# Kernel optimization log

Measured on AMD Instinct MI355X. Metric: run time of the kernel, lower is better.

Reference implementation:

```python
import jax, jax.numpy as jnp
import numpy as np

B, N, D = 8, 8192, 3
C = 64
M = 2048          # num_samples
K = 32            # max_neighbors
RADIUS = 0.3
OUT = 128
EXP = 4
CIN = C + D       # 67
HID = CIN * EXP   # 268
EPS = 1e-6        # flax LayerNorm default


def setup_inputs() -> dict:
    key = jax.random.key(0)
    ks = jax.random.split(key, 6)
    return {
        "x": jax.random.normal(ks[0], (B, N, D), jnp.float32),
        "features": jax.random.normal(ks[1], (B, N, C), jnp.float32),
        "first_idx": jax.random.randint(ks[2], (B,), 0, N, jnp.int32),
        "w1": jax.random.normal(ks[3], (CIN, HID), jnp.float32) / np.float32(np.sqrt(CIN)),
        "b1": jnp.zeros((HID,), jnp.float32),
        "g1": jnp.ones((HID,), jnp.float32),
        "be1": jnp.zeros((HID,), jnp.float32),
        "w2": jax.random.normal(ks[4], (HID, OUT), jnp.float32) / np.float32(np.sqrt(HID)),
        "b2": jnp.zeros((OUT,), jnp.float32),
        "g2": jnp.ones((OUT,), jnp.float32),
        "be2": jnp.zeros((OUT,), jnp.float32),
    }


def _layernorm(h, g, b):
    mu = jnp.mean(h, axis=-1, keepdims=True)
    var = jnp.mean(jnp.square(h), axis=-1, keepdims=True) - jnp.square(mu)
    return (h - mu) * jax.lax.rsqrt(var + EPS) * g + b


def _fps(x, first_idx, num_samples):
    # Sequential farthest-point sampling via lax.scan.
    batch = jnp.arange(x.shape[0])
    sel = jnp.full((x.shape[0], num_samples), -1, dtype=jnp.int32)
    sel = sel.at[:, 0].set(first_idx)
    first_pts = x[batch, first_idx]                       # (B,3)
    dists = jnp.sum((x - first_pts[:, None, :]) ** 2, -1)  # (B,N)

    def step(carry, i):
        s, d = carry
        far = jnp.argmax(d, axis=-1)
        s = s.at[:, i].set(far.astype(jnp.int32))
        fp = x[batch, far]
        d = jnp.minimum(d, jnp.sum((x - fp[:, None, :]) ** 2, -1))
        return (s, d), None

    (sel, _), _ = jax.lax.scan(step, (sel, dists), jnp.arange(1, num_samples))
    return sel


def _ball_query(centers, points, radius, max_neighbors):
    # centers (B,M,3), points (B,N,3) -> (B,M,K) indices, -1 where invalid
    d2 = jnp.sum((centers[:, :, None, :] - points[:, None, :, :]) ** 2, -1)  # (B,M,N)
    within = d2 < radius ** 2
    nbr = jnp.argsort(jnp.where(within, d2, 1e10), axis=-1)[:, :, :max_neighbors]
    nd = jnp.take_along_axis(d2, nbr, axis=-1)
    return jnp.where(nd < radius ** 2, nbr, -1)


def reference(x, features, first_idx, w1, b1, g1, be1, w2, b2, g2, be2):
    batch = jnp.arange(B)[:, None]                 # (B,1)
    sel = _fps(x, first_idx, M)                    # (B,M)
    centers = x[batch, sel]                        # (B,M,3)
    nbr = _ball_query(centers, x, RADIUS, K)       # (B,M,K); -1 wraps to last point (as original)
    bI = batch[:, :, None]                         # (B,1,1)
    nf = features[bI, nbr]                         # (B,M,K,C)
    npts = x[bI, nbr]                              # (B,M,K,3)
    rel = npts - centers[:, :, None, :]
    comb = jnp.concatenate([nf, rel], axis=-1)     # (B,M,K,C+3)
    h = jax.nn.gelu(comb @ w1 + b1)                # (B,M,K,HID), tanh-approx gelu as flax default
    h = _layernorm(h, g1, be1)
    h = h @ w2 + b2                                # (B,M,K,OUT)
    h = _layernorm(h, g2, be2)
    out = jnp.max(h, axis=2)                       # (B,M,OUT)
    return (centers, out)
```

## Files before the change

kernel.cpp:

```cpp
#include <hip/hip_runtime.h>
#include <hip/hip_bf16.h>
#include <math.h>

#define B_ 8
#define N_ 8192
#define C_ 64
#define M_ 2048
#define K_ 32
#define OUT_ 128
#define CIN_ 67
#define HID_ 268
#define EPS_ 1e-6f
#define CONS_ 240
#define CAPQ_ 512

typedef short short8 __attribute__((ext_vector_type(8)));
typedef float floatx4 __attribute__((ext_vector_type(4)));

__device__ __forceinline__ unsigned short f2bf(float f) {
  unsigned u = __builtin_bit_cast(unsigned, f);
  u += 0x7fffu + ((u >> 16) & 1u);
  return (unsigned short)(u >> 16);
}
__device__ __forceinline__ float bf2f(unsigned short h) {
  return __builtin_bit_cast(float, (unsigned)h << 16);
}

__device__ __forceinline__ float d2fma(float ax, float ay, float az,
                                       float bx, float by, float bz) {
#pragma clang fp contract(off)
  float dx = ax - bx, dy = ay - by, dz = az - bz;
  return __builtin_fmaf(dz, dz, __builtin_fmaf(dy, dy, dx * dx));
}

__device__ __forceinline__ float gelu_tanh(float v) {
  const float k0 = 0.7978845608028654f;
  const float k1 = 0.044715f;
  float u = k0 * (v + k1 * v * v * v);
  return 0.5f * v * (1.0f + tanhf(u));
}

__device__ __forceinline__ int msp4(int v) {
  return (v & 1) | ((v & 2) << 2) | ((v & 4) << 4) | ((v & 8) << 6);
}

template <int CTRL>
__device__ __forceinline__ unsigned long long dpp_umax64(unsigned long long k) {
  int lo = (int)(unsigned)k;
  int hi = (int)(unsigned)(k >> 32);
  unsigned slo = (unsigned)__builtin_amdgcn_update_dpp(0, lo, CTRL, 0xF, 0xF, true);
  unsigned shi = (unsigned)__builtin_amdgcn_update_dpp(0, hi, CTRL, 0xF, 0xF, true);
  unsigned long long o = ((unsigned long long)shi << 32) | (unsigned long long)slo;
  return k > o ? k : o;
}

__global__ __launch_bounds__(256) void pack_kernel(
    const float* __restrict__ w1, const float* __restrict__ w2,
    unsigned short* __restrict__ w1p, unsigned short* __restrict__ w2p,
    int* __restrict__ prog) {
  if (blockIdx.x == 0) prog[threadIdx.x] = 0;
  int e = blockIdx.x * 256 + threadIdx.x;
  if (e < 3 * 17 * 64 * 8) {
    int j = e & 7, lane = (e >> 3) & 63, fi = e >> 9;
    int kt = fi / 17, nt = fi - kt * 17;
    int k = kt * 32 + (lane >> 4) * 8 + j;
    int n = nt * 16 + (lane & 15);
    float v = (k < CIN_ && n < HID_) ? w1[k * HID_ + n] : 0.f;
    w1p[e] = f2bf(v);
  } else {
    int e2 = e - 3 * 17 * 64 * 8;
    if (e2 < 9 * 8 * 64 * 8) {
      int j = e2 & 7, lane = (e2 >> 3) & 63, fi = e2 >> 9;
      int kt = fi >> 3, nt = fi & 7;
      int k = kt * 32 + (lane >> 4) * 8 + j;
      int n = nt * 16 + (lane & 15);
      float v = (k < HID_) ? w2[k * OUT_ + n] : 0.f;
      w2p[e2] = f2bf(v);
    }
  }
}

__global__ __launch_bounds__(512) void fused_kernel(
    const float* __restrict__ x, const float* __restrict__ features,
    const int* __restrict__ first_idx,
    const unsigned short* __restrict__ w1p, const float* __restrict__ b1,
    const float* __restrict__ g1, const float* __restrict__ be1,
    const unsigned short* __restrict__ w2p, const float* __restrict__ b2,
    const float* __restrict__ g2, const float* __restrict__ be2,
    float* __restrict__ centers, float* __restrict__ out1,
    int* __restrict__ prog) {
  __shared__ __align__(16) char smem[131456];
  const int tid = threadIdx.x;
  const int lane = tid & 63;
  const int wv = tid >> 6;

  if (blockIdx.x < B_) {
    const int b = blockIdx.x;
    const float* xb = x + (size_t)b * N_ * 3;

    float* s_xyz = (float*)smem;
    char* s_mem = smem + 98304;
    unsigned long long* s_wkey = (unsigned long long*)(smem + 131072);
    int* s_wsum = (int*)(smem + 131200);
    float* s_bb = (float*)(smem + 131232);

    int* s_hist = (int*)s_mem;
    unsigned short* s_perm = (unsigned short*)(s_mem + 16384);
    float* s_cbuf = (float*)s_mem;

    {
      const float4* src = (const float4*)xb;
      float4* dst = (float4*)s_xyz;
#pragma unroll
      for (int i = 0; i < 12; ++i) {
        int e = tid + i * 512;
        dst[e] = src[e];
      }
    }
    for (int i = tid; i < 4096; i += 512) s_hist[i] = 0;
    __syncthreads();

    float bx0 = INFINITY, bx1 = -INFINITY, by0 = INFINITY, by1 = -INFINITY,
          bz0 = INFINITY, bz1 = -INFINITY;
#pragma unroll
    for (int i = 0; i < 16; ++i) {
      int p = tid + i * 512;
      float X = s_xyz[p * 3 + 0], Y = s_xyz[p * 3 + 1], Z = s_xyz[p * 3 + 2];
      bx0 = fminf(bx0, X); bx1 = fmaxf(bx1, X);
      by0 = fminf(by0, Y); by1 = fmaxf(by1, Y);
      bz0 = fminf(bz0, Z); bz1 = fmaxf(bz1, Z);
    }
#pragma unroll
    for (int off = 1; off < 64; off <<= 1) {
      bx0 = fminf(bx0, __shfl_xor(bx0, off)); bx1 = fmaxf(bx1, __shfl_xor(bx1, off));
      by0 = fminf(by0, __shfl_xor(by0, off)); by1 = fmaxf(by1, __shfl_xor(by1, off));
      bz0 = fminf(bz0, __shfl_xor(bz0, off)); bz1 = fmaxf(bz1, __shfl_xor(bz1, off));
    }
    if (lane == 0) {
      s_bb[wv * 6 + 0] = bx0; s_bb[wv * 6 + 1] = bx1; s_bb[wv * 6 + 2] = by0;
      s_bb[wv * 6 + 3] = by1; s_bb[wv * 6 + 4] = bz0; s_bb[wv * 6 + 5] = bz1;
    }
    __syncthreads();
#pragma unroll
    for (int w = 0; w < 8; ++w) {
      bx0 = fminf(bx0, s_bb[w * 6 + 0]); bx1 = fmaxf(bx1, s_bb[w * 6 + 1]);
      by0 = fminf(by0, s_bb[w * 6 + 2]); by1 = fmaxf(by1, s_bb[w * 6 + 3]);
      bz0 = fminf(bz0, s_bb[w * 6 + 4]); bz1 = fmaxf(bz1, s_bb[w * 6 + 5]);
    }
    const float kS = 16.0f * (1.0f - 1e-6f);
    float rx = bx1 - bx0, ry = by1 - by0, rz = bz1 - bz0;
    float sxv = rx > 0.f ? kS / rx : 0.f;
    float syv = ry > 0.f ? kS / ry : 0.f;
    float szv = rz > 0.f ? kS / rz : 0.f;

#pragma unroll
    for (int i = 0; i < 16; ++i) {
      int p = tid + i * 512;
      int qx = (int)((s_xyz[p * 3 + 0] - bx0) * sxv);
      int qy = (int)((s_xyz[p * 3 + 1] - by0) * syv);
      int qz = (int)((s_xyz[p * 3 + 2] - bz0) * szv);
      qx = qx < 0 ? 0 : (qx > 15 ? 15 : qx);
      qy = qy < 0 ? 0 : (qy > 15 ? 15 : qy);
      qz = qz < 0 ? 0 : (qz > 15 ? 15 : qz);
      int c = msp4(qx) | (msp4(qy) << 1) | (msp4(qz) << 2);
      atomicAdd(&s_hist[c], 1);
    }
    __syncthreads();

    {
      int h[8], pre[8];
      int acc = 0;
#pragma unroll
      for (int i = 0; i < 8; ++i) { h[i] = s_hist[tid * 8 + i]; pre[i] = acc; acc += h[i]; }
      int incl = acc;
#pragma unroll
      for (int off = 1; off < 64; off <<= 1) {
        int v = __shfl_up(incl, off);
        if (lane >= off) incl += v;
      }
      int texcl = incl - acc;
      if (lane == 63) s_wsum[wv] = incl;
      __syncthreads();
      int woff = 0;
#pragma unroll
      for (int w = 0; w < 8; ++w) woff += (w < wv) ? s_wsum[w] : 0;
#pragma unroll
      for (int i = 0; i < 8; ++i) s_hist[tid * 8 + i] = woff + texcl + pre[i];
    }
    __syncthreads();

#pragma unroll
    for (int i = 0; i < 16; ++i) {
      int p = tid + i * 512;
      int qx = (int)((s_xyz[p * 3 + 0] - bx0) * sxv);
      int qy = (int)((s_xyz[p * 3 + 1] - by0) * syv);
      int qz = (int)((s_xyz[p * 3 + 2] - bz0) * szv);
      qx = qx < 0 ? 0 : (qx > 15 ? 15 : qx);
      qy = qy < 0 ? 0 : (qy > 15 ? 15 : qy);
      qz = qz < 0 ? 0 : (qz > 15 ? 15 : qz);
      int c = msp4(qx) | (msp4(qy) << 1) | (msp4(qz) << 2);
      int pos = atomicAdd(&s_hist[c], 1);
      s_perm[pos] = (unsigned short)p;
    }
    __syncthreads();

    float px[16], py[16], pz[16], d[16];
    unsigned lo32[16];
    float gx0[2], gx1[2], gy0[2], gy1[2], gz0[2], gz1[2];
#pragma unroll
    for (int g = 0; g < 2; ++g) {
      gx0[g] = INFINITY; gx1[g] = -INFINITY; gy0[g] = INFINITY;
      gy1[g] = -INFINITY; gz0[g] = INFINITY; gz1[g] = -INFINITY;
    }
#pragma unroll
    for (int i = 0; i < 16; ++i) {
      int p = (int)s_perm[tid * 16 + i];
      int g = i >> 3;
      px[i] = s_xyz[p * 3 + 0];
      py[i] = s_xyz[p * 3 + 1];
      pz[i] = s_xyz[p * 3 + 2];
      d[i] = INFINITY;
      lo32[i] = 0xFFFFFFFFu - (unsigned)p;
      gx0[g] = fminf(gx0[g], px[i]); gx1[g] = fmaxf(gx1[g], px[i]);
      gy0[g] = fminf(gy0[g], py[i]); gy1[g] = fmaxf(gy1[g], py[i]);
      gz0[g] = fminf(gz0[g], pz[i]); gz1[g] = fmaxf(gz1[g], pz[i]);
    }
    float wx0 = fminf(gx0[0], gx0[1]), wx1 = fmaxf(gx1[0], gx1[1]);
    float wy0 = fminf(gy0[0], gy0[1]), wy1 = fmaxf(gy1[0], gy1[1]);
    float wz0 = fminf(gz0[0], gz0[1]), wz1 = fmaxf(gz1[0], gz1[1]);
#pragma unroll
    for (int off = 1; off < 64; off <<= 1) {
      wx0 = fminf(wx0, __shfl_xor(wx0, off)); wx1 = fmaxf(wx1, __shfl_xor(wx1, off));
      wy0 = fminf(wy0, __shfl_xor(wy0, off)); wy1 = fmaxf(wy1, __shfl_xor(wy1, off));
      wz0 = fminf(wz0, __shfl_xor(wz0, off)); wz1 = fmaxf(wz1, __shfl_xor(wz1, off));
    }

    int fi = first_idx[b];
    float ncx = s_xyz[fi * 3 + 0], ncy = s_xyz[fi * 3 + 1], ncz = s_xyz[fi * 3 + 2];
    if (tid == 0) {
      s_cbuf[0] = ncx; s_cbuf[1] = ncy; s_cbuf[2] = ncz;
    }

    unsigned long long gkey[2];
    gkey[0] = 0x7F800000ULL << 32;
    gkey[1] = 0x7F800000ULL << 32;
    unsigned long long wk = 0x7F800000ULL << 32;

    for (int it = 1; it < M_; ++it) {
      float wdx = fmaxf(fmaxf(wx0 - ncx, ncx - wx1), 0.f);
      float wdy = fmaxf(fmaxf(wy0 - ncy, ncy - wy1), 0.f);
      float wdz = fmaxf(fmaxf(wz0 - ncz, ncz - wz1), 0.f);
      float wlb = __builtin_fmaf(wdz, wdz, __builtin_fmaf(wdy, wdy, wdx * wdx));
      float wgm = __builtin_bit_cast(float, (unsigned)(wk >> 32));
      if (__any(wlb * 0.999f < wgm)) {
#pragma unroll
        for (int g = 0; g < 2; ++g) {
          float gdx = fmaxf(fmaxf(gx0[g] - ncx, ncx - gx1[g]), 0.f);
          float gdy = fmaxf(fmaxf(gy0[g] - ncy, ncy - gy1[g]), 0.f);
          float gdz = fmaxf(fmaxf(gz0[g] - ncz, ncz - gz1[g]), 0.f);
          float glb = __builtin_fmaf(gdz, gdz, __builtin_fmaf(gdy, gdy, gdx * gdx));
          float ggm = __builtin_bit_cast(float, (unsigned)(gkey[g] >> 32));
          if (glb * 0.999f < ggm) {
            unsigned long long k[8];
#pragma unroll
            for (int i = 0; i < 8; ++i) {
              int s = g * 8 + i;
              float dd = d2fma(px[s], py[s], pz[s], ncx, ncy, ncz);
              float dm = fminf(d[s], dd);
              d[s] = dm;
              k[i] = ((unsigned long long)__builtin_bit_cast(unsigned, dm) << 32) |
                     (unsigned long long)lo32[s];
            }
#pragma unroll
            for (int sd = 4; sd >= 1; sd >>= 1)
#pragma unroll
              for (int i = 0; i < sd; ++i)
                k[i] = k[i] > k[i + sd] ? k[i] : k[i + sd];
            gkey[g] = k[0];
          }
        }
        unsigned long long kk = gkey[0] > gkey[1] ? gkey[0] : gkey[1];
        kk = dpp_umax64<0x111>(kk);
        kk = dpp_umax64<0x112>(kk);
        kk = dpp_umax64<0x114>(kk);
        kk = dpp_umax64<0x118>(kk);
        kk = dpp_umax64<0x142>(kk);
        kk = dpp_umax64<0x143>(kk);
        wk = kk;
      }
      if (lane == 63) s_wkey[(it & 1) * 8 + wv] = wk;
      __syncthreads();
      if ((it & 31) == 0) {
        if (wv == 0 && lane < 24) {
          const float4* src = (const float4*)(s_cbuf + (size_t)(it - 32) * 3);
          float4* dst = (float4*)(centers + (size_t)b * M_ * 3 + (size_t)(it - 32) * 3);
          dst[lane] = src[lane];
        }
        if (tid == 0)
          __hip_atomic_store(&prog[b * 32], it, __ATOMIC_RELEASE, __HIP_MEMORY_SCOPE_AGENT);
      }
      {
        const ulonglong2* sp = (const ulonglong2*)(&s_wkey[(it & 1) * 8]);
        ulonglong2 q0 = sp[0], q1 = sp[1], q2 = sp[2], q3 = sp[3];
        unsigned long long a0 = q0.x > q0.y ? q0.x : q0.y;
        unsigned long long a1 = q1.x > q1.y ? q1.x : q1.y;
        unsigned long long a2 = q2.x > q2.y ? q2.x : q2.y;
        unsigned long long a3 = q3.x > q3.y ? q3.x : q3.y;
        unsigned long long b0 = a0 > a1 ? a0 : a1;
        unsigned long long b1v = a2 > a3 ? a2 : a3;
        unsigned long long gk = b0 > b1v ? b0 : b1v;
        int gi = (int)(0xFFFFFFFFu - (unsigned)(gk & 0xFFFFFFFFull));
        int gs = __builtin_amdgcn_readfirstlane(gi);
        ncx = s_xyz[gs * 3 + 0];
        ncy = s_xyz[gs * 3 + 1];
        ncz = s_xyz[gs * 3 + 2];
      }
      if (tid == 0) {
        s_cbuf[it * 3 + 0] = ncx; s_cbuf[it * 3 + 1] = ncy; s_cbuf[it * 3 + 2] = ncz;
      }
    }

    __syncthreads();
    if (wv == 0 && lane < 24) {
      const float4* src = (const float4*)(s_cbuf + (size_t)(M_ - 32) * 3);
      float4* dst = (float4*)(centers + (size_t)b * M_ * 3 + (size_t)(M_ - 32) * 3);
      dst[lane] = src[lane];
    }
    if (tid == 0)
      __hip_atomic_store(&prog[b * 32], M_, __ATOMIC_RELEASE, __HIP_MEMORY_SCOPE_AGENT);

  } else {
    unsigned short* A1 = (unsigned short*)smem;
    unsigned short* H1 = (unsigned short*)(smem + 13312);
    float* H2 = (float*)(smem + 51200);
    float* cd = (float*)(smem + 84992);
    int* cidx = (int*)(smem + 89088);
    float* s_sum = (float*)(smem + 93184);
    float* s_sum2 = (float*)(smem + 93440);
    float* s_mu = (float*)(smem + 93696);
    float* s_rs = (float*)(smem + 93952);
    int* s_nbr = (int*)(smem + 94208);
    float* s_ctr = (float*)(smem + 94464);
    int* s_wc = (int*)(smem + 94496);

    const int j = (int)blockIdx.x - B_;
    const int b = j & 7;
    const int c = j >> 3;
    const int q4 = lane >> 4;
    const int nl = lane & 15;

    for (int e = tid; e < 64 * 104; e += 512) A1[e] = 0;
    for (int e = tid; e < 64 * 296; e += 512) H1[e] = 0;
    __syncthreads();

    const float* xb = x + (size_t)b * N_ * 3;

    for (int k35 = 0; k35 < 35; ++k35) {
      int i = c + 30 * k35;
      if (i >= 1024) break;
      const int m0 = 2 * i, m1 = m0 + 1;
      const int cm0 = b * M_ + m0;

      if (tid == 0) {
        if (__hip_atomic_load(&prog[b * 32], __ATOMIC_ACQUIRE,
                              __HIP_MEMORY_SCOPE_AGENT) <= m1) {
          do {
            __builtin_amdgcn_s_sleep(16);
          } while (__hip_atomic_load(&prog[b * 32], __ATOMIC_ACQUIRE,
                                     __HIP_MEMORY_SCOPE_AGENT) <= m1);
        }
      }
      __syncthreads();

      if (tid < 64) s_sum[tid] = 0.f;
      else if (tid < 128) s_sum2[tid - 64] = 0.f;
      else if (tid < 134) s_ctr[tid - 128] = centers[(size_t)cm0 * 3 + (tid - 128)];
      __syncthreads();

      const float c0x = s_ctr[0], c0y = s_ctr[1], c0z = s_ctr[2];
      const float c1x = s_ctr[3], c1y = s_ctr[4], c1z = s_ctr[5];

      int cnt0 = 0, cnt1 = 0;
      for (int s = 0; s < 16; ++s) {
        int p = wv * 1024 + s * 64 + lane;
        float X = xb[p * 3 + 0], Y = xb[p * 3 + 1], Z = xb[p * 3 + 2];
        float d20 = d2fma(X, Y, Z, c0x, c0y, c0z);
        float d21 = d2fma(X, Y, Z, c1x, c1y, c1z);
        cnt0 += (int)__popcll(__ballot(d20 < 0.09f));
        cnt1 += (int)__popcll(__ballot(d21 < 0.09f));
      }
      if (lane == 0) { s_wc[wv] = cnt0; s_wc[8 + wv] = cnt1; }
      __syncthreads();
      int base0 = 0, tot0 = 0, base1 = 0, tot1 = 0;
#pragma unroll
      for (int w = 0; w < 8; ++w) {
        int v0 = s_wc[w], v1 = s_wc[8 + w];
        base0 += (w < wv) ? v0 : 0; tot0 += v0;
        base1 += (w < wv) ? v1 : 0; tot1 += v1;
      }
      int count0 = tot0 < CAPQ_ ? tot0 : CAPQ_;
      int count1 = tot1 < CAPQ_ ? tot1 : CAPQ_;
      int pos0 = base0, pos1 = base1;
      for (int s = 0; s < 16; ++s) {
        int p = wv * 1024 + s * 64 + lane;
        float X = xb[p * 3 + 0], Y = xb[p * 3 + 1], Z = xb[p * 3 + 2];
        float d20 = d2fma(X, Y, Z, c0x, c0y, c0z);
        float d21 = d2fma(X, Y, Z, c1x, c1y, c1z);
        bool in0 = d20 < 0.09f;
        bool in1 = d21 < 0.09f;
        unsigned long long m0m = __ballot(in0);
        unsigned long long m1m = __ballot(in1);
        if (in0) {
          int pp = pos0 + (int)__popcll(m0m & ((1ull << lane) - 1ull));
          if (pp < CAPQ_) { cd[pp] = d20; cidx[pp] = p; }
        }
        if (in1) {
          int pp = pos1 + (int)__popcll(m1m & ((1ull << lane) - 1ull));
          if (pp < CAPQ_) { cd[CAPQ_ + pp] = d21; cidx[CAPQ_ + pp] = p; }
        }
        pos0 += (int)__popcll(m0m);
        pos1 += (int)__popcll(m1m);
      }
      __syncthreads();
      {
        int q = tid >> 8;
        int lt = tid & 255;
        int cnt = q ? count1 : count0;
        int nw = cnt < K_ ? cnt : K_;
        const float* cdq = cd + q * CAPQ_;
        const int* cxq = cidx + q * CAPQ_;
        for (int cc = lt; cc < cnt; cc += 256) {
          float dcc = cdq[cc];
          int rank = 0;
          for (int jj = 0; jj < cnt; ++jj) {
            float dj = cdq[jj];
            rank += (dj < dcc || (dj == dcc && jj < cc)) ? 1 : 0;
          }
          if (rank < K_) s_nbr[q * K_ + rank] = cxq[cc];
        }
        for (int s = nw + lt; s < K_; s += 256) s_nbr[q * K_ + s] = N_ - 1;
      }
      __syncthreads();

#pragma unroll
      for (int h = 0; h < 2; ++h) {
        int rr = (tid >> 4) + h * 32;
        int jj = tid & 15;
        int q = rr >> 5;
        int idx = s_nbr[rr];
        const float4* frow = (const float4*)(features + ((size_t)b * N_ + idx) * C_);
        float4 f4 = frow[jj];
        int base = rr * 104 + jj * 4;
        A1[base + 0] = f2bf(f4.x); A1[base + 1] = f2bf(f4.y);
        A1[base + 2] = f2bf(f4.z); A1[base + 3] = f2bf(f4.w);
        if (jj == 0) {
          const float* xp = x + ((size_t)b * N_ + idx) * 3;
          A1[rr * 104 + 64] = f2bf(xp[0] - s_ctr[q * 3 + 0]);
          A1[rr * 104 + 65] = f2bf(xp[1] - s_ctr[q * 3 + 1]);
          A1[rr * 104 + 66] = f2bf(xp[2] - s_ctr[q * 3 + 2]);
        }
      }
      __syncthreads();

      for (int nt = wv; nt < 17; nt += 8) {
        short8 bfr[3];
#pragma unroll
        for (int kt = 0; kt < 3; ++kt)
          bfr[kt] = *(const short8*)(w1p + (size_t)((kt * 17 + nt) * 64 + lane) * 8);
        int col = nt * 16 + nl;
        bool cok = col < HID_;
        float bias = cok ? b1[col] : 0.f;
#pragma unroll
        for (int mt = 0; mt < 4; ++mt) {
          floatx4 acc = {0.f, 0.f, 0.f, 0.f};
          const unsigned short* ap = A1 + (mt * 16 + nl) * 104 + q4 * 8;
#pragma unroll
          for (int kt = 0; kt < 3; ++kt) {
            short8 a = *(const short8*)(ap + kt * 32);
            acc = __builtin_amdgcn_mfma_f32_16x16x32_bf16(a, bfr[kt], acc, 0, 0, 0);
          }
#pragma unroll
          for (int r = 0; r < 4; ++r) {
            int row = mt * 16 + q4 * 4 + r;
            float g = 0.f;
            if (cok) {
              float v = acc[r] + bias;
              g = gelu_tanh(v);
              H1[row * 296 + col] = f2bf(g);
            }
            float s1 = g, s2 = g * g;
#pragma unroll
            for (int off = 1; off < 16; off <<= 1) {
              s1 += __shfl_xor(s1, off);
              s2 += __shfl_xor(s2, off);
            }
            if (nl == 0) { atomicAdd(&s_sum[row], s1); atomicAdd(&s_sum2[row], s2); }
          }
        }
      }
      __syncthreads();
      if (tid < 64) {
        float mu = s_sum[tid] * (1.f / HID_);
        float var = s_sum2[tid] * (1.f / HID_) - mu * mu;
        s_mu[tid] = mu;
        s_rs[tid] = rsqrtf(var + EPS_);
      }
      __syncthreads();
      for (int e = tid; e < 64 * HID_; e += 512) {
        int r = e / HID_, cc = e - r * HID_;
        float g = bf2f(H1[r * 296 + cc]);
        float v = (g - s_mu[r]) * s_rs[r] * g1[cc] + be1[cc];
        H1[r * 296 + cc] = f2bf(v);
      }
      if (tid < 64) { s_sum[tid] = 0.f; s_sum2[tid] = 0.f; }
      __syncthreads();

      {
        int nt = wv;
        short8 bfr2[9];
#pragma unroll
        for (int kt = 0; kt < 9; ++kt)
          bfr2[kt] = *(const short8*)(w2p + (size_t)((kt * 8 + nt) * 64 + lane) * 8);
        int col = nt * 16 + nl;
        float bias = b2[col];
#pragma unroll
        for (int mt = 0; mt < 4; ++mt) {
          floatx4 acc = {0.f, 0.f, 0.f, 0.f};
          const unsigned short* ap = H1 + (mt * 16 + nl) * 296 + q4 * 8;
#pragma unroll
          for (int kt = 0; kt < 9; ++kt) {
            short8 a = *(const short8*)(ap + kt * 32);
            acc = __builtin_amdgcn_mfma_f32_16x16x32_bf16(a, bfr2[kt], acc, 0, 0, 0);
          }
#pragma unroll
          for (int r = 0; r < 4; ++r) {
            int row = mt * 16 + q4 * 4 + r;
            float v = acc[r] + bias;
            H2[row * 132 + col] = v;
            float s1 = v, s2 = v * v;
#pragma unroll
            for (int off = 1; off < 16; off <<= 1) {
              s1 += __shfl_xor(s1, off);
              s2 += __shfl_xor(s2, off);
            }
            if (nl == 0) { atomicAdd(&s_sum[row], s1); atomicAdd(&s_sum2[row], s2); }
          }
        }
      }
      __syncthreads();
      if (tid < 64) {
        float mu = s_sum[tid] * (1.f / OUT_);
        float var = s_sum2[tid] * (1.f / OUT_) - mu * mu;
        s_mu[tid] = mu;
        s_rs[tid] = rsqrtf(var + EPS_);
      }
      __syncthreads();
      if (tid < 256) {
        int q = tid >> 7, col = tid & 127;
        float gg = g2[col], bb = be2[col];
        float mx = -3.4e38f;
#pragma unroll 4
        for (int r = 0; r < K_; ++r) {
          int row = q * K_ + r;
          float v = H2[row * 132 + col];
          float o = (v - s_mu[row]) * s_rs[row] * gg + bb;
          mx = fmaxf(mx, o);
        }
        out1[(size_t)(cm0 + q) * OUT_ + col] = mx;
      }
      __syncthreads();
    }
  }
}

extern "C" void kernel_launch(void* const* d_in, const int* in_sizes, int n_in,
                              void* d_out, int out_size, void* d_ws, size_t ws_size,
                              hipStream_t stream) {
  const float* x = (const float*)d_in[0];
  const float* features = (const float*)d_in[1];
  const int* first_idx = (const int*)d_in[2];
  const float* w1 = (const float*)d_in[3];
  const float* b1 = (const float*)d_in[4];
  const float* g1 = (const float*)d_in[5];
  const float* be1 = (const float*)d_in[6];
  const float* w2 = (const float*)d_in[7];
  const float* b2 = (const float*)d_in[8];
  const float* g2 = (const float*)d_in[9];
  const float* be2 = (const float*)d_in[10];

  float* centers = (float*)d_out;
  float* out1 = (float*)d_out + (size_t)B_ * M_ * 3;

  int* prog = (int*)d_ws;
  unsigned short* w1p = (unsigned short*)((char*)d_ws + 2097152);
  unsigned short* w2p = (unsigned short*)((char*)d_ws + 2149376);

  pack_kernel<<<dim3(246), dim3(256), 0, stream>>>(w1, w2, w1p, w2p, prog);
  fused_kernel<<<dim3(B_ + CONS_), dim3(512), 0, stream>>>(
      x, features, first_idx, w1p, b1, g1, be1, w2p, b2, g2, be2,
      centers, out1, prog);
}
```

Before: 1.943 ms.

## Emit two FPS samples per iteration via top-2 reduction when second stays farthest

The farthest-point-sampling loop now tracks the top-2 keys per group, wave and block instead of only the max. When the runner-up point is still at least as far from the new winner as its stored distance, both are accepted in one iteration, which roughly halves the block-wide barriers on the sequential critical path. Consumer polling also switches to relaxed loads with a longer sleep and atomic reads of centers. The cost is extra work for the 64-bit top-2 merges. The relaxed ordering may weaken the producer-consumer memory guarantees.

```diff
diff --git a/kernel.cpp b/kernel.cpp
--- a/kernel.cpp
+++ b/kernel.cpp
@@ -16,6 +16,7 @@
 
 typedef short short8 __attribute__((ext_vector_type(8)));
 typedef float floatx4 __attribute__((ext_vector_type(4)));
+typedef unsigned long long ull;
 
 __device__ __forceinline__ unsigned short f2bf(float f) {
   unsigned u = __builtin_bit_cast(unsigned, f);
@@ -44,14 +45,38 @@
   return (v & 1) | ((v & 2) << 2) | ((v & 4) << 4) | ((v & 8) << 6);
 }
 
+__device__ __forceinline__ void top2_merge(ull &a1, ull &a2, ull b1, ull b2) {
+  bool c = a1 > b1;
+  ull h = c ? a1 : b1;
+  ull l = c ? b1 : a1;
+  ull s = c ? a2 : b2;
+  ull sec = l > s ? l : s;
+  a1 = h; a2 = sec;
+}
+
 template <int CTRL>
-__device__ __forceinline__ unsigned long long dpp_umax64(unsigned long long k) {
+__device__ __forceinline__ ull dpp_mov64(ull k) {
   int lo = (int)(unsigned)k;
   int hi = (int)(unsigned)(k >> 32);
   unsigned slo = (unsigned)__builtin_amdgcn_update_dpp(0, lo, CTRL, 0xF, 0xF, true);
   unsigned shi = (unsigned)__builtin_amdgcn_update_dpp(0, hi, CTRL, 0xF, 0xF, true);
-  unsigned long long o = ((unsigned long long)shi << 32) | (unsigned long long)slo;
-  return k > o ? k : o;
+  return ((ull)shi << 32) | (ull)slo;
+}
+
+template <int CTRL>
+__device__ __forceinline__ void dpp_top2(ull &a1, ull &a2) {
+  ull b1 = dpp_mov64<CTRL>(a1);
+  ull b2 = dpp_mov64<CTRL>(a2);
+  top2_merge(a1, a2, b1, b2);
+}
+
+__device__ __forceinline__ void wave_dpp_top2(ull &k1, ull &k2) {
+  dpp_top2<0x111>(k1, k2);
+  dpp_top2<0x112>(k1, k2);
+  dpp_top2<0x114>(k1, k2);
+  dpp_top2<0x118>(k1, k2);
+  dpp_top2<0x142>(k1, k2);
+  dpp_top2<0x143>(k1, k2);
 }
 
 __global__ __launch_bounds__(256) void pack_kernel(
@@ -89,7 +114,7 @@
     const float* __restrict__ g2, const float* __restrict__ be2,
     float* __restrict__ centers, float* __restrict__ out1,
     int* __restrict__ prog) {
-  __shared__ __align__(16) char smem[131456];
+  __shared__ __align__(16) char smem[133632];
   const int tid = threadIdx.x;
   const int lane = tid & 63;
   const int wv = tid >> 6;
@@ -100,9 +125,9 @@
 
     float* s_xyz = (float*)smem;
     char* s_mem = smem + 98304;
-    unsigned long long* s_wkey = (unsigned long long*)(smem + 131072);
-    int* s_wsum = (int*)(smem + 131200);
-    float* s_bb = (float*)(smem + 131232);
+    ulonglong2* s_went = (ulonglong2*)(smem + 131072);
+    int* s_wsum = (int*)(smem + 131328);
+    float* s_bb = (float*)(smem + 131360);
 
     int* s_hist = (int*)s_mem;
     unsigned short* s_perm = (unsigned short*)(s_mem + 16384);
@@ -225,109 +250,142 @@
       gy0[g] = fminf(gy0[g], py[i]); gy1[g] = fmaxf(gy1[g], py[i]);
       gz0[g] = fminf(gz0[g], pz[i]); gz1[g] = fmaxf(gz1[g], pz[i]);
     }
-    float wx0 = fminf(gx0[0], gx0[1]), wx1 = fmaxf(gx1[0], gx1[1]);
-    float wy0 = fminf(gy0[0], gy0[1]), wy1 = fmaxf(gy1[0], gy1[1]);
-    float wz0 = fminf(gz0[0], gz0[1]), wz1 = fmaxf(gz1[0], gz1[1]);
-#pragma unroll
-    for (int off = 1; off < 64; off <<= 1) {
-      wx0 = fminf(wx0, __shfl_xor(wx0, off)); wx1 = fmaxf(wx1, __shfl_xor(wx1, off));
-      wy0 = fminf(wy0, __shfl_xor(wy0, off)); wy1 = fmaxf(wy1, __shfl_xor(wy1, off));
-      wz0 = fminf(wz0, __shfl_xor(wz0, off)); wz1 = fmaxf(wz1, __shfl_xor(wz1, off));
-    }
 
     int fi = first_idx[b];
-    float ncx = s_xyz[fi * 3 + 0], ncy = s_xyz[fi * 3 + 1], ncz = s_xyz[fi * 3 + 2];
-    if (tid == 0) {
-      s_cbuf[0] = ncx; s_cbuf[1] = ncy; s_cbuf[2] = ncz;
-    }
-
-    unsigned long long gkey[2];
-    gkey[0] = 0x7F800000ULL << 32;
-    gkey[1] = 0x7F800000ULL << 32;
-    unsigned long long wk = 0x7F800000ULL << 32;
-
-    for (int it = 1; it < M_; ++it) {
-      float wdx = fmaxf(fmaxf(wx0 - ncx, ncx - wx1), 0.f);
-      float wdy = fmaxf(fmaxf(wy0 - ncy, ncy - wy1), 0.f);
-      float wdz = fmaxf(fmaxf(wz0 - ncz, ncz - wz1), 0.f);
-      float wlb = __builtin_fmaf(wdz, wdz, __builtin_fmaf(wdy, wdy, wdx * wdx));
-      float wgm = __builtin_bit_cast(float, (unsigned)(wk >> 32));
-      if (__any(wlb * 0.999f < wgm)) {
+    float c0x = s_xyz[fi * 3 + 0], c0y = s_xyz[fi * 3 + 1], c0z = s_xyz[fi * 3 + 2];
+    float c1x = 0.f, c1y = 0.f, c1z = 0.f;
+    int npend = 1;
+    int produced = 1;
+    int nf = 0;
+    if (tid == 0) { s_cbuf[0] = c0x; s_cbuf[1] = c0y; s_cbuf[2] = c0z; }
+
+    ull gk1[2], gk2[2];
+    gk1[0] = gk1[1] = gk2[0] = gk2[1] = 0x7F800000ULL << 32;
+    ull wk1 = gk1[0], wk2 = gk1[0];
+    int par = 0;
+
+    for (;;) {
+      par ^= 1;
+      if (produced < M_) {
+        bool t1[2], t2[2];
+        bool anyt = false;
 #pragma unroll
         for (int g = 0; g < 2; ++g) {
-          float gdx = fmaxf(fmaxf(gx0[g] - ncx, ncx - gx1[g]), 0.f);
-          float gdy = fmaxf(fmaxf(gy0[g] - ncy, ncy - gy1[g]), 0.f);
-          float gdz = fmaxf(fmaxf(gz0[g] - ncz, ncz - gz1[g]), 0.f);
-          float glb = __builtin_fmaf(gdz, gdz, __builtin_fmaf(gdy, gdy, gdx * gdx));
-          float ggm = __builtin_bit_cast(float, (unsigned)(gkey[g] >> 32));
-          if (glb * 0.999f < ggm) {
-            unsigned long long k[8];
-#pragma unroll
-            for (int i = 0; i < 8; ++i) {
-              int s = g * 8 + i;
-              float dd = d2fma(px[s], py[s], pz[s], ncx, ncy, ncz);
-              float dm = fminf(d[s], dd);
-              d[s] = dm;
-              k[i] = ((unsigned long long)__builtin_bit_cast(unsigned, dm) << 32) |
-                     (unsigned long long)lo32[s];
+          float ggm = __builtin_bit_cast(float, (unsigned)(gk1[g] >> 32));
+          float a = fmaxf(fmaxf(gx0[g] - c0x, c0x - gx1[g]), 0.f);
+          float bq = fmaxf(fmaxf(gy0[g] - c0y, c0y - gy1[g]), 0.f);
+          float cq = fmaxf(fmaxf(gz0[g] - c0z, c0z - gz1[g]), 0.f);
+          float lb0 = __builtin_fmaf(cq, cq, __builtin_fmaf(bq, bq, a * a));
+          t1[g] = lb0 * 0.999f < ggm;
+          t2[g] = false;
+          if (npend == 2) {
+            float a2 = fmaxf(fmaxf(gx0[g] - c1x, c1x - gx1[g]), 0.f);
+            float b2q = fmaxf(fmaxf(gy0[g] - c1y, c1y - gy1[g]), 0.f);
+            float c2q = fmaxf(fmaxf(gz0[g] - c1z, c1z - gz1[g]), 0.f);
+            float lb1 = __builtin_fmaf(c2q, c2q, __builtin_fmaf(b2q, b2q, a2 * a2));
+            t2[g] = lb1 * 0.999f < ggm;
+          }
+          anyt = anyt || t1[g] || t2[g];
+        }
+        if (__any(anyt)) {
+#pragma unroll
+          for (int g = 0; g < 2; ++g) {
+            if (t1[g] || t2[g]) {
+              ull k[8];
+#pragma unroll
+              for (int i = 0; i < 8; ++i) {
+                int s = g * 8 + i;
+                float dm = d[s];
+                if (t1[g]) dm = fminf(dm, d2fma(px[s], py[s], pz[s], c0x, c0y, c0z));
+                if (t2[g]) dm = fminf(dm, d2fma(px[s], py[s], pz[s], c1x, c1y, c1z));
+                d[s] = dm;
+                k[i] = ((ull)__builtin_bit_cast(unsigned, dm) << 32) | (ull)lo32[s];
+              }
+              ull m0 = k[0] > k[1] ? k[0] : k[1], n0 = k[0] > k[1] ? k[1] : k[0];
+              ull m1 = k[2] > k[3] ? k[2] : k[3], n1 = k[2] > k[3] ? k[3] : k[2];
+              ull m2 = k[4] > k[5] ? k[4] : k[5], n2 = k[4] > k[5] ? k[5] : k[4];
+              ull m3 = k[6] > k[7] ? k[6] : k[7], n3 = k[6] > k[7] ? k[7] : k[6];
+              top2_merge(m0, n0, m1, n1);
+              top2_merge(m2, n2, m3, n3);
+              top2_merge(m0, n0, m2, n2);
+              gk1[g] = m0; gk2[g] = n0;
             }
-#pragma unroll
-            for (int sd = 4; sd >= 1; sd >>= 1)
-#pragma unroll
-              for (int i = 0; i < sd; ++i)
-                k[i] = k[i] > k[i + sd] ? k[i] : k[i + sd];
-            gkey[g] = k[0];
-          }
-        }
-        unsigned long long kk = gkey[0] > gkey[1] ? gkey[0] : gkey[1];
-        kk = dpp_umax64<0x111>(kk);
-        kk = dpp_umax64<0x112>(kk);
-        kk = dpp_umax64<0x114>(kk);
-        kk = dpp_umax64<0x118>(kk);
-        kk = dpp_umax64<0x142>(kk);
-        kk = dpp_umax64<0x143>(kk);
-        wk = kk;
-      }
-      if (lane == 63) s_wkey[(it & 1) * 8 + wv] = wk;
-      __syncthreads();
-      if ((it & 31) == 0) {
-        if (wv == 0 && lane < 24) {
-          const float4* src = (const float4*)(s_cbuf + (size_t)(it - 32) * 3);
-          float4* dst = (float4*)(centers + (size_t)b * M_ * 3 + (size_t)(it - 32) * 3);
+          }
+          ull a1 = gk1[0], a2 = gk2[0];
+          top2_merge(a1, a2, gk1[1], gk2[1]);
+          wave_dpp_top2(a1, a2);
+          wk1 = a1; wk2 = a2;
+        }
+        if (lane == 63) {
+          ulonglong2 sl; sl.x = wk1; sl.y = wk2;
+          s_went[par * 8 + wv] = sl;
+        }
+      }
+      __syncthreads();
+      if (produced >= M_) break;
+
+      ull K1, K2;
+      {
+        const ulonglong2* sp = &s_went[par * 8];
+        ulonglong2 s0 = sp[0];
+        K1 = s0.x; K2 = s0.y;
+#pragma unroll
+        for (int w = 1; w < 8; ++w) {
+          ulonglong2 sw = sp[w];
+          top2_merge(K1, K2, sw.x, sw.y);
+        }
+      }
+      int i1 = (int)(0xFFFFFFFFu - (unsigned)(K1 & 0xFFFFFFFFull));
+      int i2 = (int)(0xFFFFFFFFu - (unsigned)(K2 & 0xFFFFFFFFull));
+      int u1 = __builtin_amdgcn_readfirstlane(i1);
+      int u2 = __builtin_amdgcn_readfirstlane(i2);
+      float w1x = s_xyz[u1 * 3 + 0], w1y = s_xyz[u1 * 3 + 1], w1z = s_xyz[u1 * 3 + 2];
+      float rxx = s_xyz[u2 * 3 + 0], ryy = s_xyz[u2 * 3 + 1], rzz = s_xyz[u2 * 3 + 2];
+      float dR = __builtin_bit_cast(float, (unsigned)(K2 >> 32));
+      float dd = d2fma(rxx, ryy, rzz, w1x, w1y, w1z);
+      bool two = (dd >= dR) && (produced + 2 <= M_);
+      if (tid == 0) {
+        s_cbuf[produced * 3 + 0] = w1x;
+        s_cbuf[produced * 3 + 1] = w1y;
+        s_cbuf[produced * 3 + 2] = w1z;
+        if (two) {
+          s_cbuf[produced * 3 + 3] = rxx;
+          s_cbuf[produced * 3 + 4] = ryy;
+          s_cbuf[produced * 3 + 5] = rzz;
+        }
+      }
+      produced += two ? 2 : 1;
+      c0x = w1x; c0y = w1y; c0z = w1z;
+      if (two) { c1x = rxx; c1y = ryy; c1z = rzz; npend = 2; }
+      else npend = 1;
+      if (wv == 0) {
+        while (nf + 32 <= produced) {
+          if (lane < 24) {
+            const float4* src = (const float4*)(s_cbuf + (size_t)nf * 3);
+            float4* dst = (float4*)(centers + (size_t)b * M_ * 3 + (size_t)nf * 3);
+            dst[lane] = src[lane];
+          }
+          nf += 32;
+          if (lane == 0)
+            __hip_atomic_store(&prog[b * 32], nf, __ATOMIC_RELEASE,
+                               __HIP_MEMORY_SCOPE_AGENT);
+        }
+      }
+    }
+
+    if (wv == 0) {
+      while (nf < M_) {
+        if (lane < 24) {
+          const float4* src = (const float4*)(s_cbuf + (size_t)nf * 3);
+          float4* dst = (float4*)(centers + (size_t)b * M_ * 3 + (size_t)nf * 3);
           dst[lane] = src[lane];
         }
-        if (tid == 0)
-          __hip_atomic_store(&prog[b * 32], it, __ATOMIC_RELEASE, __HIP_MEMORY_SCOPE_AGENT);
-      }
-      {
-        const ulonglong2* sp = (const ulonglong2*)(&s_wkey[(it & 1) * 8]);
-        ulonglong2 q0 = sp[0], q1 = sp[1], q2 = sp[2], q3 = sp[3];
-        unsigned long long a0 = q0.x > q0.y ? q0.x : q0.y;
-        unsigned long long a1 = q1.x > q1.y ? q1.x : q1.y;
-        unsigned long long a2 = q2.x > q2.y ? q2.x : q2.y;
-        unsigned long long a3 = q3.x > q3.y ? q3.x : q3.y;
-        unsigned long long b0 = a0 > a1 ? a0 : a1;
-        unsigned long long b1v = a2 > a3 ? a2 : a3;
-        unsigned long long gk = b0 > b1v ? b0 : b1v;
-        int gi = (int)(0xFFFFFFFFu - (unsigned)(gk & 0xFFFFFFFFull));
-        int gs = __builtin_amdgcn_readfirstlane(gi);
-        ncx = s_xyz[gs * 3 + 0];
-        ncy = s_xyz[gs * 3 + 1];
-        ncz = s_xyz[gs * 3 + 2];
-      }
-      if (tid == 0) {
-        s_cbuf[it * 3 + 0] = ncx; s_cbuf[it * 3 + 1] = ncy; s_cbuf[it * 3 + 2] = ncz;
-      }
-    }
-
-    __syncthreads();
-    if (wv == 0 && lane < 24) {
-      const float4* src = (const float4*)(s_cbuf + (size_t)(M_ - 32) * 3);
-      float4* dst = (float4*)(centers + (size_t)b * M_ * 3 + (size_t)(M_ - 32) * 3);
-      dst[lane] = src[lane];
-    }
-    if (tid == 0)
-      __hip_atomic_store(&prog[b * 32], M_, __ATOMIC_RELEASE, __HIP_MEMORY_SCOPE_AGENT);
+        nf += 32;
+      }
+      if (lane == 0)
+        __hip_atomic_store(&prog[b * 32], M_, __ATOMIC_RELEASE,
+                           __HIP_MEMORY_SCOPE_AGENT);
+    }
 
   } else {
     unsigned short* A1 = (unsigned short*)smem;
@@ -362,19 +420,20 @@
       const int cm0 = b * M_ + m0;
 
       if (tid == 0) {
-        if (__hip_atomic_load(&prog[b * 32], __ATOMIC_ACQUIRE,
-                              __HIP_MEMORY_SCOPE_AGENT) <= m1) {
-          do {
-            __builtin_amdgcn_s_sleep(16);
-          } while (__hip_atomic_load(&prog[b * 32], __ATOMIC_ACQUIRE,
-                                     __HIP_MEMORY_SCOPE_AGENT) <= m1);
-        }
+        while (__hip_atomic_load(&prog[b * 32], __ATOMIC_RELAXED,
+                                 __HIP_MEMORY_SCOPE_AGENT) <= m1)
+          __builtin_amdgcn_s_sleep(32);
       }
       __syncthreads();
 
       if (tid < 64) s_sum[tid] = 0.f;
       else if (tid < 128) s_sum2[tid - 64] = 0.f;
-      else if (tid < 134) s_ctr[tid - 128] = centers[(size_t)cm0 * 3 + (tid - 128)];
+      else if (tid < 134) {
+        unsigned wrd = __hip_atomic_load(
+            (const unsigned*)&centers[(size_t)cm0 * 3 + (tid - 128)],
+            __ATOMIC_RELAXED, __HIP_MEMORY_SCOPE_AGENT);
+        s_ctr[tid - 128] = __builtin_bit_cast(float, wrd);
+      }
       __syncthreads();
 
       const float c0x = s_ctr[0], c0y = s_ctr[1], c0z = s_ctr[2];
@@ -443,8 +502,8 @@
       __syncthreads();
 
 #pragma unroll
-      for (int h = 0; h < 2; ++h) {
-        int rr = (tid >> 4) + h * 32;
+      for (int hh = 0; hh < 2; ++hh) {
+        int rr = (tid >> 4) + hh * 32;
         int jj = tid & 15;
         int q = rr >> 5;
         int idx = s_nbr[rr];
```

After: 2.795 ms. 43.9% more time.

## Drop wave-level FPS bbox cull, cache ball-query distances, relax spin wait

Applied to the files above, without the earlier changes.

In the FPS loop, the wave-wide bounding-box pre-test is removed and each lane now checks its two point groups' bounds directly, with one wave vote. This saves a shuffle reduction at setup and a test per iteration, but the per-group test now runs every iteration. In the ball-query stage, the squared distances from the counting pass are kept in registers and reused in the compaction pass, so coordinates are not reloaded and distances not recomputed. The progress spin-wait now uses relaxed loads with a longer sleep, and center values are read with relaxed atomic loads, which may weaken producer/consumer ordering.

```diff
diff --git a/kernel.cpp b/kernel.cpp
--- a/kernel.cpp
+++ b/kernel.cpp
@@ -52,6 +52,16 @@
   unsigned shi = (unsigned)__builtin_amdgcn_update_dpp(0, hi, CTRL, 0xF, 0xF, true);
   unsigned long long o = ((unsigned long long)shi << 32) | (unsigned long long)slo;
   return k > o ? k : o;
+}
+
+__device__ __forceinline__ unsigned long long wave_dpp_max64(unsigned long long kk) {
+  kk = dpp_umax64<0x111>(kk);
+  kk = dpp_umax64<0x112>(kk);
+  kk = dpp_umax64<0x114>(kk);
+  kk = dpp_umax64<0x118>(kk);
+  kk = dpp_umax64<0x142>(kk);
+  kk = dpp_umax64<0x143>(kk);
+  return kk;
 }
 
 __global__ __launch_bounds__(256) void pack_kernel(
@@ -225,15 +235,6 @@
       gy0[g] = fminf(gy0[g], py[i]); gy1[g] = fmaxf(gy1[g], py[i]);
       gz0[g] = fminf(gz0[g], pz[i]); gz1[g] = fmaxf(gz1[g], pz[i]);
     }
-    float wx0 = fminf(gx0[0], gx0[1]), wx1 = fmaxf(gx1[0], gx1[1]);
-    float wy0 = fminf(gy0[0], gy0[1]), wy1 = fmaxf(gy1[0], gy1[1]);
-    float wz0 = fminf(gz0[0], gz0[1]), wz1 = fmaxf(gz1[0], gz1[1]);
-#pragma unroll
-    for (int off = 1; off < 64; off <<= 1) {
-      wx0 = fminf(wx0, __shfl_xor(wx0, off)); wx1 = fmaxf(wx1, __shfl_xor(wx1, off));
-      wy0 = fminf(wy0, __shfl_xor(wy0, off)); wy1 = fmaxf(wy1, __shfl_xor(wy1, off));
-      wz0 = fminf(wz0, __shfl_xor(wz0, off)); wz1 = fmaxf(wz1, __shfl_xor(wz1, off));
-    }
 
     int fi = first_idx[b];
     float ncx = s_xyz[fi * 3 + 0], ncy = s_xyz[fi * 3 + 1], ncz = s_xyz[fi * 3 + 2];
@@ -247,20 +248,20 @@
     unsigned long long wk = 0x7F800000ULL << 32;
 
     for (int it = 1; it < M_; ++it) {
-      float wdx = fmaxf(fmaxf(wx0 - ncx, ncx - wx1), 0.f);
-      float wdy = fmaxf(fmaxf(wy0 - ncy, ncy - wy1), 0.f);
-      float wdz = fmaxf(fmaxf(wz0 - ncz, ncz - wz1), 0.f);
-      float wlb = __builtin_fmaf(wdz, wdz, __builtin_fmaf(wdy, wdy, wdx * wdx));
-      float wgm = __builtin_bit_cast(float, (unsigned)(wk >> 32));
-      if (__any(wlb * 0.999f < wgm)) {
+      bool tr[2];
+#pragma unroll
+      for (int g = 0; g < 2; ++g) {
+        float gdx = fmaxf(fmaxf(gx0[g] - ncx, ncx - gx1[g]), 0.f);
+        float gdy = fmaxf(fmaxf(gy0[g] - ncy, ncy - gy1[g]), 0.f);
+        float gdz = fmaxf(fmaxf(gz0[g] - ncz, ncz - gz1[g]), 0.f);
+        float glb = __builtin_fmaf(gdz, gdz, __builtin_fmaf(gdy, gdy, gdx * gdx));
+        float ggm = __builtin_bit_cast(float, (unsigned)(gkey[g] >> 32));
+        tr[g] = glb * 0.999f < ggm;
+      }
+      if (__any(tr[0] || tr[1])) {
 #pragma unroll
         for (int g = 0; g < 2; ++g) {
-          float gdx = fmaxf(fmaxf(gx0[g] - ncx, ncx - gx1[g]), 0.f);
-          float gdy = fmaxf(fmaxf(gy0[g] - ncy, ncy - gy1[g]), 0.f);
-          float gdz = fmaxf(fmaxf(gz0[g] - ncz, ncz - gz1[g]), 0.f);
-          float glb = __builtin_fmaf(gdz, gdz, __builtin_fmaf(gdy, gdy, gdx * gdx));
-          float ggm = __builtin_bit_cast(float, (unsigned)(gkey[g] >> 32));
-          if (glb * 0.999f < ggm) {
+          if (tr[g]) {
             unsigned long long k[8];
 #pragma unroll
             for (int i = 0; i < 8; ++i) {
@@ -280,13 +281,7 @@
           }
         }
         unsigned long long kk = gkey[0] > gkey[1] ? gkey[0] : gkey[1];
-        kk = dpp_umax64<0x111>(kk);
-        kk = dpp_umax64<0x112>(kk);
-        kk = dpp_umax64<0x114>(kk);
-        kk = dpp_umax64<0x118>(kk);
-        kk = dpp_umax64<0x142>(kk);
-        kk = dpp_umax64<0x143>(kk);
-        wk = kk;
+        wk = wave_dpp_max64(kk);
       }
       if (lane == 63) s_wkey[(it & 1) * 8 + wv] = wk;
       __syncthreads();
@@ -362,32 +357,35 @@
       const int cm0 = b * M_ + m0;
 
       if (tid == 0) {
-        if (__hip_atomic_load(&prog[b * 32], __ATOMIC_ACQUIRE,
-                              __HIP_MEMORY_SCOPE_AGENT) <= m1) {
-          do {
-            __builtin_amdgcn_s_sleep(16);
-          } while (__hip_atomic_load(&prog[b * 32], __ATOMIC_ACQUIRE,
-                                     __HIP_MEMORY_SCOPE_AGENT) <= m1);
-        }
+        while (__hip_atomic_load(&prog[b * 32], __ATOMIC_RELAXED,
+                                 __HIP_MEMORY_SCOPE_AGENT) <= m1)
+          __builtin_amdgcn_s_sleep(32);
       }
       __syncthreads();
 
       if (tid < 64) s_sum[tid] = 0.f;
       else if (tid < 128) s_sum2[tid - 64] = 0.f;
-      else if (tid < 134) s_ctr[tid - 128] = centers[(size_t)cm0 * 3 + (tid - 128)];
+      else if (tid < 134) {
+        unsigned wrd = __hip_atomic_load(
+            (const unsigned*)&centers[(size_t)cm0 * 3 + (tid - 128)],
+            __ATOMIC_RELAXED, __HIP_MEMORY_SCOPE_AGENT);
+        s_ctr[tid - 128] = __builtin_bit_cast(float, wrd);
+      }
       __syncthreads();
 
       const float c0x = s_ctr[0], c0y = s_ctr[1], c0z = s_ctr[2];
       const float c1x = s_ctr[3], c1y = s_ctr[4], c1z = s_ctr[5];
 
+      float d20c[16], d21c[16];
       int cnt0 = 0, cnt1 = 0;
+#pragma unroll
       for (int s = 0; s < 16; ++s) {
         int p = wv * 1024 + s * 64 + lane;
         float X = xb[p * 3 + 0], Y = xb[p * 3 + 1], Z = xb[p * 3 + 2];
-        float d20 = d2fma(X, Y, Z, c0x, c0y, c0z);
-        float d21 = d2fma(X, Y, Z, c1x, c1y, c1z);
-        cnt0 += (int)__popcll(__ballot(d20 < 0.09f));
-        cnt1 += (int)__popcll(__ballot(d21 < 0.09f));
+        d20c[s] = d2fma(X, Y, Z, c0x, c0y, c0z);
+        d21c[s] = d2fma(X, Y, Z, c1x, c1y, c1z);
+        cnt0 += (int)__popcll(__ballot(d20c[s] < 0.09f));
+        cnt1 += (int)__popcll(__ballot(d21c[s] < 0.09f));
       }
       if (lane == 0) { s_wc[wv] = cnt0; s_wc[8 + wv] = cnt1; }
       __syncthreads();
@@ -401,11 +399,10 @@
       int count0 = tot0 < CAPQ_ ? tot0 : CAPQ_;
       int count1 = tot1 < CAPQ_ ? tot1 : CAPQ_;
       int pos0 = base0, pos1 = base1;
+#pragma unroll
       for (int s = 0; s < 16; ++s) {
         int p = wv * 1024 + s * 64 + lane;
-        float X = xb[p * 3 + 0], Y = xb[p * 3 + 1], Z = xb[p * 3 + 2];
-        float d20 = d2fma(X, Y, Z, c0x, c0y, c0z);
-        float d21 = d2fma(X, Y, Z, c1x, c1y, c1z);
+        float d20 = d20c[s], d21 = d21c[s];
         bool in0 = d20 < 0.09f;
         bool in1 = d21 < 0.09f;
         unsigned long long m0m = __ballot(in0);
@@ -443,8 +440,8 @@
       __syncthreads();
 
 #pragma unroll
-      for (int h = 0; h < 2; ++h) {
-        int rr = (tid >> 4) + h * 32;
+      for (int hh = 0; hh < 2; ++hh) {
+        int rr = (tid >> 4) + hh * 32;
         int jj = tid & 15;
         int q = rr >> 5;
         int idx = s_nbr[rr];
```

After: 1.894 ms (median of 2 runs). -2.5%, faster.
